# Performance work log

Measured on AMD Instinct MI355X. Metric: run time of the kernel, lower is better.

Reference implementation:

```python
import jax, jax.numpy as jnp
import numpy as np
from jax import lax

# Dims matching init_kwargs
T, BK, OBS = 2048, 64, 64   # obs_dim = percept_dim(63) + reward_dim(1)
H, P, N = 16, 64, 64        # nheads, headdim, d_state; d_inner = H*P = 1024
DIN = H * P


def setup_inputs() -> dict:
    key = jax.random.key(0)
    ks = jax.random.split(key, 12)
    s = lambda fan_in: 1.0 / np.sqrt(fan_in)
    return {
        "obs": jax.random.normal(ks[0], (T, BK, OBS), jnp.float32),
        "reward": jax.random.normal(ks[1], (T, BK, 1), jnp.float32),
        "W_in": jax.random.normal(ks[2], (OBS, DIN), jnp.float32) * s(OBS),
        "W_B": jax.random.normal(ks[3], (OBS, N), jnp.float32) * s(OBS),
        "W_C": jax.random.normal(ks[4], (OBS, N), jnp.float32) * s(OBS),
        "W_dt": jax.random.normal(ks[5], (1, H), jnp.float32),
        "dt_bias": jax.random.normal(ks[6], (H,), jnp.float32) * 0.5,
        "A_log": jax.random.uniform(ks[7], (H,), jnp.float32, 0.0, 1.0),
        "D": jax.random.normal(ks[8], (H,), jnp.float32),
        "W_out": jax.random.normal(ks[9], (DIN, 1), jnp.float32) * s(DIN),
        "init_state": jax.random.normal(ks[10], (H, P, N), jnp.float32) * 0.1,
        "k": 8,
    }


def reference(obs, reward, W_in, W_B, W_C, W_dt, dt_bias, A_log, D, W_out, init_state, k):
    # obs: (T, Bk, obs_dim), reward: (T, Bk, 1)
    Tn, Bk, _ = obs.shape
    # Precompute per-step projections (vectorized over time)
    u = (obs @ W_in).reshape(Tn, Bk, H, P)      # (T,Bk,H,P) input stream
    Bm = obs @ W_B                              # (T,Bk,N) input-dependent B
    Cm = obs @ W_C                              # (T,Bk,N) input-dependent C
    dt = jax.nn.softplus(reward @ W_dt + dt_bias)  # (T,Bk,H) reward-modulated dt
    A = -jnp.exp(A_log)                          # (H,) negative decay rates
    decay = jnp.exp(dt * A)                     # (T,Bk,H)

    # Cache init: zeros + initial_states (per QAgent.forward)
    h0 = jnp.broadcast_to(init_state, (Bk, H, P, N))

    def step(h, inp):
        u_t, B_t, C_t, dt_t, dec_t = inp
        # selective-scan state update: h = h*exp(dt*A) + dt*u (outer) B
        h = h * dec_t[..., None, None] + (dt_t[..., None] * u_t)[..., None] * B_t[:, None, None, :]
        y = jnp.einsum('bhpn,bn->bhp', h, C_t) + D[None, :, None] * u_t
        o = y.reshape(Bk, DIN) @ W_out          # (Bk, 1) scalar Q per option
        return h, o

    _, ys = lax.scan(step, h0, (u, Bm, Cm, dt, decay))  # ys: (T, Bk, 1)
    q = ys.reshape(Tn, -1, k)                   # (T, B, k)
    logits = q
    return q, logits
```

## Files before the change

kernel.cpp:

```cpp
#include <hip/hip_runtime.h>
#include <math.h>

#define TT     2048
#define BKK    64
#define OBSD   64
#define NH     16
#define PDIM   64
#define NSTATE 64
#define DINN   1024
#define TB     (TT*BKK)
#define DDS    32
#define BCS    128

template <int CTRL>
__device__ __forceinline__ float dpp_add(float x) {
    int y = __builtin_amdgcn_update_dpp(0, __float_as_int(x), CTRL, 0xF, 0xF, true);
    return x + __int_as_float(y);
}
__device__ __forceinline__ float wave_sum_lane63(float x) {
    x = dpp_add<0x111>(x);
    x = dpp_add<0x112>(x);
    x = dpp_add<0x114>(x);
    x = dpp_add<0x118>(x);
    x = dpp_add<0x142>(x);
    x = dpp_add<0x143>(x);
    return x;
}

__device__ __forceinline__ float softplusf(float z) {
    return (z > 20.f) ? z : log1pf(expf(z));
}

#define LOAD_DX(ptr, dd_, xx_)                                            \
    {                                                                     \
        const float4* _p = (const float4*)(ptr);                          \
        float4 a0 = _p[0], a1 = _p[1], a2 = _p[2], a3 = _p[3];            \
        float4 b0 = _p[4], b1 = _p[5], b2 = _p[6], b3 = _p[7];            \
        dd_[0]=a0.x; dd_[1]=a0.y; dd_[2]=a0.z; dd_[3]=a0.w;               \
        dd_[4]=a1.x; dd_[5]=a1.y; dd_[6]=a1.z; dd_[7]=a1.w;               \
        dd_[8]=a2.x; dd_[9]=a2.y; dd_[10]=a2.z; dd_[11]=a2.w;             \
        dd_[12]=a3.x; dd_[13]=a3.y; dd_[14]=a3.z; dd_[15]=a3.w;           \
        xx_[0]=b0.x; xx_[1]=b0.y; xx_[2]=b0.z; xx_[3]=b0.w;               \
        xx_[4]=b1.x; xx_[5]=b1.y; xx_[6]=b1.z; xx_[7]=b1.w;               \
        xx_[8]=b2.x; xx_[9]=b2.y; xx_[10]=b2.z; xx_[11]=b2.w;             \
        xx_[12]=b3.x; xx_[13]=b3.y; xx_[14]=b3.z; xx_[15]=b3.w;           \
    }

__global__ __launch_bounds__(256)
void init_proj2(const float* __restrict__ Win, const float* __restrict__ Wout,
                const float* __restrict__ initS,
                float* __restrict__ wproj, float* __restrict__ g0) {
    const int t = threadIdx.x;
    if (blockIdx.x < 4) {
        const int idx = blockIdx.x * 256 + t;
        const int k = idx >> 4, h = idx & 15;
        float s = 0.f;
#pragma unroll 8
        for (int p = 0; p < PDIM; ++p)
            s = fmaf(Win[(size_t)k * DINN + h * 64 + p], Wout[h * 64 + p], s);
        wproj[idx] = s;
    } else {
        const int idx = (blockIdx.x - 4) * 256 + t;
        const int h = idx >> 6, n = idx & 63;
        float s = 0.f;
#pragma unroll 8
        for (int p = 0; p < PDIM; ++p)
            s = fmaf(initS[h * PDIM * NSTATE + p * NSTATE + n], Wout[h * 64 + p], s);
        g0[idx] = s;
    }
}

__global__ __launch_bounds__(256)
void bc_gemm(const float* __restrict__ obs, const float* __restrict__ WB,
             const float* __restrict__ WC, float* __restrict__ BC) {
    __shared__ float tile[128 * OBSD];

    const int t = threadIdx.x;
    const size_t r0 = (size_t)blockIdx.x * 128;

    {
        const float4* src = (const float4*)(obs + r0 * OBSD);
        float4* dst = (float4*)tile;
#pragma unroll
        for (int i = 0; i < 8; ++i)
            dst[i * 256 + t] = src[i * 256 + t];
    }
    __syncthreads();

    const int lane = t & 63;
    const int w = __builtin_amdgcn_readfirstlane(t >> 6);

    float wb[64], wc[64];
#pragma unroll
    for (int k = 0; k < 64; ++k) wb[k] = WB[k * 64 + lane];
#pragma unroll
    for (int k = 0; k < 64; ++k) wc[k] = WC[k * 64 + lane];

    const float* trow = tile + w * 32 * OBSD;
    float* brow = BC + (r0 + w * 32) * BCS;

#pragma unroll 1
    for (int r = 0; r < 32; ++r) {
        const float4* tr4 = (const float4*)(trow + r * OBSD);
        float s0 = 0.f, s1 = 0.f, s2 = 0.f, s3 = 0.f;
        float c0 = 0.f, c1 = 0.f, c2 = 0.f, c3 = 0.f;
#pragma unroll
        for (int kq = 0; kq < 16; ++kq) {
            const float4 o = tr4[kq];
            const int k = kq * 4;
            s0 = fmaf(o.x, wb[k],     s0);  c0 = fmaf(o.x, wc[k],     c0);
            s1 = fmaf(o.y, wb[k + 1], s1);  c1 = fmaf(o.y, wc[k + 1], c1);
            s2 = fmaf(o.z, wb[k + 2], s2);  c2 = fmaf(o.z, wc[k + 2], c2);
            s3 = fmaf(o.w, wb[k + 3], s3);  c3 = fmaf(o.w, wc[k + 3], c3);
        }
        brow[lane]      = (s0 + s1) + (s2 + s3);
        brow[64 + lane] = (c0 + c1) + (c2 + c3);
        brow += BCS;
    }
}

__global__ __launch_bounds__(256)
void prelude3(const float* __restrict__ obs, const float* __restrict__ reward,
              const float* __restrict__ Wdt, const float* __restrict__ dtb,
              const float* __restrict__ Alog, const float* __restrict__ Dv,
              const float* __restrict__ wproj, float* __restrict__ dd,
              float* __restrict__ obw) {
    int gw = (blockIdx.x * 256 + threadIdx.x) >> 6;
    gw = __builtin_amdgcn_readfirstlane(gw);
    const int lane = threadIdx.x & 63;
    const int row0 = gw * 8;
    if (row0 >= TB) return;

    const int h = lane & 15;
    const int q = lane >> 4;

    const float wdt_h = Wdt[h];
    const float dtb_h = dtb[h];
    const float A_h   = -expf(Alog[h]);
    const float D_h   = Dv[h];
    float wpj[16];
#pragma unroll
    for (int j = 0; j < 16; ++j)
        wpj[j] = wproj[(q * 16 + j) * 16 + h];

#pragma unroll 1
    for (int r = 0; r < 8; ++r) {
        const int row = row0 + r;

        const float4* oq = (const float4*)(obs + (size_t)row * OBSD + q * 16);
        float4 o0 = oq[0], o1 = oq[1], o2 = oq[2], o3 = oq[3];
        float wpart = 0.f;
        wpart = fmaf(o0.x, wpj[0],  wpart); wpart = fmaf(o0.y, wpj[1],  wpart);
        wpart = fmaf(o0.z, wpj[2],  wpart); wpart = fmaf(o0.w, wpj[3],  wpart);
        wpart = fmaf(o1.x, wpj[4],  wpart); wpart = fmaf(o1.y, wpj[5],  wpart);
        wpart = fmaf(o1.z, wpj[6],  wpart); wpart = fmaf(o1.w, wpj[7],  wpart);
        wpart = fmaf(o2.x, wpj[8],  wpart); wpart = fmaf(o2.y, wpj[9],  wpart);
        wpart = fmaf(o2.z, wpj[10], wpart); wpart = fmaf(o2.w, wpj[11], wpart);
        wpart = fmaf(o3.x, wpj[12], wpart); wpart = fmaf(o3.y, wpj[13], wpart);
        wpart = fmaf(o3.z, wpj[14], wpart); wpart = fmaf(o3.w, wpj[15], wpart);
        wpart += __shfl_xor(wpart, 16, 64);
        wpart += __shfl_xor(wpart, 32, 64);

        const float rew  = reward[row];
        const float dtv  = softplusf(fmaf(rew, wdt_h, dtb_h));
        const float decv = expf(dtv * A_h);
        const float xwv  = dtv * wpart;

        float* dr = dd + (size_t)row * DDS;
        if (q == 0) dr[h]      = decv;
        if (q == 1) dr[16 + h] = xwv;

        float dw = D_h * wpart;
        dw += __shfl_xor(dw, 1, 64);
        dw += __shfl_xor(dw, 2, 64);
        dw += __shfl_xor(dw, 4, 64);
        dw += __shfl_xor(dw, 8, 64);
        if (lane == 0) obw[row] = dw;
    }
}

template <int NCT>
__global__ __launch_bounds__(256)
void phaseA(const float* __restrict__ BC, const float* __restrict__ dd,
            float* __restrict__ Send, float* __restrict__ Ptot) {
    const int CLT = TT / NCT;
    int w = blockIdx.x * 4 + (threadIdx.x >> 6);
    w = __builtin_amdgcn_readfirstlane(w);
    const int lane = threadIdx.x & 63;
    const int b = w & 63;
    const int c = w >> 6;

    const float* bp = BC + ((size_t)(c * CLT) * BKK + b) * BCS;
    const float* dr = dd + ((size_t)(c * CLT) * BKK + b) * DDS;

    float g[16], Pc[16];
#pragma unroll
    for (int hh = 0; hh < 16; ++hh) { g[hh] = 0.f; Pc[hh] = 1.f; }

    float Bv = bp[lane];
    float dec_[16], xw_[16];
    LOAD_DX(dr, dec_, xw_);

#pragma unroll 2
    for (int i = 0; i < CLT; ++i) {
        const float* bn = bp + (size_t)BKK * BCS;
        const float* dn = dr + (size_t)BKK * DDS;
        float Bn = 0.f;
        float decn_[16], xwn_[16];
        if (i < CLT - 1) {
            Bn = bn[lane];
            LOAD_DX(dn, decn_, xwn_);
        }
#pragma unroll
        for (int hh = 0; hh < 16; ++hh) {
            g[hh] = fmaf(g[hh], dec_[hh], xw_[hh] * Bv);
            Pc[hh] *= dec_[hh];
        }
        bp = bn; dr = dn; Bv = Bn;
        if (i < CLT - 1) {
#pragma unroll
            for (int hh = 0; hh < 16; ++hh) { dec_[hh] = decn_[hh]; xw_[hh] = xwn_[hh]; }
        }
    }

    const size_t base = ((size_t)c * BKK + b) * 16;
#pragma unroll
    for (int hh = 0; hh < 16; ++hh)
        Send[(base + hh) * 64 + lane] = g[hh];
    if (lane == 0) {
#pragma unroll
        for (int hh = 0; hh < 16; ++hh)
            Ptot[base + hh] = Pc[hh];
    }
}

template <int NCT>
__global__ __launch_bounds__(64)
void phaseB(const float* __restrict__ g0, const float* __restrict__ Send,
            const float* __restrict__ Ptot, float* __restrict__ gcbuf) {
    const int b    = blockIdx.x;
    const int lane = threadIdx.x;

    float g[16];
#pragma unroll
    for (int hh = 0; hh < 16; ++hh)
        g[hh] = g0[hh * 64 + lane];

    float S_[16], P_[16];
    {
        const size_t base = (size_t)b * 16;
#pragma unroll
        for (int hh = 0; hh < 16; ++hh) S_[hh] = Send[(base + hh) * 64 + lane];
        const float4* pp = (const float4*)(Ptot + base);
        float4 a0 = pp[0], a1 = pp[1], a2 = pp[2], a3 = pp[3];
        P_[0]=a0.x; P_[1]=a0.y; P_[2]=a0.z; P_[3]=a0.w;
        P_[4]=a1.x; P_[5]=a1.y; P_[6]=a1.z; P_[7]=a1.w;
        P_[8]=a2.x; P_[9]=a2.y; P_[10]=a2.z; P_[11]=a2.w;
        P_[12]=a3.x; P_[13]=a3.y; P_[14]=a3.z; P_[15]=a3.w;
    }

#pragma unroll 1
    for (int c = 0; c < NCT; ++c) {
        const size_t base = ((size_t)c * BKK + b) * 16;
        float Sn[16], Pn[16];
        if (c < NCT - 1) {
            const size_t nb = ((size_t)(c + 1) * BKK + b) * 16;
#pragma unroll
            for (int hh = 0; hh < 16; ++hh) Sn[hh] = Send[(nb + hh) * 64 + lane];
            const float4* pp = (const float4*)(Ptot + nb);
            float4 a0 = pp[0], a1 = pp[1], a2 = pp[2], a3 = pp[3];
            Pn[0]=a0.x; Pn[1]=a0.y; Pn[2]=a0.z; Pn[3]=a0.w;
            Pn[4]=a1.x; Pn[5]=a1.y; Pn[6]=a1.z; Pn[7]=a1.w;
            Pn[8]=a2.x; Pn[9]=a2.y; Pn[10]=a2.z; Pn[11]=a2.w;
            Pn[12]=a3.x; Pn[13]=a3.y; Pn[14]=a3.z; Pn[15]=a3.w;
        }
#pragma unroll
        for (int hh = 0; hh < 16; ++hh)
            gcbuf[(base + hh) * 64 + lane] = g[hh];
        if (c < NCT - 1) {
#pragma unroll
            for (int hh = 0; hh < 16; ++hh) {
                g[hh] = fmaf(P_[hh], g[hh], S_[hh]);
                P_[hh] = Pn[hh]; S_[hh] = Sn[hh];
            }
        }
    }
}

template <int NCT>
__global__ __launch_bounds__(256)
void phaseC(const float* __restrict__ BC, const float* __restrict__ dd,
            const float* __restrict__ obw, const float* __restrict__ gcbuf,
            float* __restrict__ qout) {
    const int CLT = TT / NCT;
    int w = blockIdx.x * 4 + (threadIdx.x >> 6);
    w = __builtin_amdgcn_readfirstlane(w);
    const int lane = threadIdx.x & 63;
    const int b = w & 63;
    const int c = w >> 6;

    const size_t sbase = ((size_t)c * BKK + b) * 16;
    float g[16];
#pragma unroll
    for (int hh = 0; hh < 16; ++hh)
        g[hh] = gcbuf[(sbase + hh) * 64 + lane];

    const float* bp = BC  + ((size_t)(c * CLT) * BKK + b) * BCS;
    const float* dr = dd  + ((size_t)(c * CLT) * BKK + b) * DDS;
    const float* op = obw + ((size_t)(c * CLT) * BKK + b);

    float Bv = bp[lane];
    float Cv = bp[64 + lane];
    float ob = op[0];
    float dec_[16], xw_[16];
    LOAD_DX(dr, dec_, xw_);

#pragma unroll 2
    for (int i = 0; i < CLT; ++i) {
        const float* bn = bp + (size_t)BKK * BCS;
        const float* dn = dr + (size_t)BKK * DDS;
        const float* on = op + (size_t)BKK;
        float Bn = 0.f, Cn = 0.f, obn = 0.f;
        float decn_[16], xwn_[16];
        if (i < CLT - 1) {
            Bn = bn[lane]; Cn = bn[64 + lane]; obn = on[0];
            LOAD_DX(dn, decn_, xwn_);
        }

        float y = 0.f;
#pragma unroll
        for (int hh = 0; hh < 16; ++hh) {
            g[hh] = fmaf(g[hh], dec_[hh], xw_[hh] * Bv);
            y = fmaf(g[hh], Cv, y);
        }

        float tot = wave_sum_lane63(y);
        if (lane == 63) {
            const size_t idx = (size_t)(c * CLT + i) * BKK + b;
            const float v = tot + ob;
            qout[idx]      = v;
            qout[TB + idx] = v;
        }

        bp = bn; dr = dn; op = on;
        Bv = Bn; Cv = Cn; ob = obn;
        if (i < CLT - 1) {
#pragma unroll
            for (int hh = 0; hh < 16; ++hh) { dec_[hh] = decn_[hh]; xw_[hh] = xwn_[hh]; }
        }
    }
}

extern "C" void kernel_launch(void* const* d_in, const int* in_sizes, int n_in,
                              void* d_out, int out_size, void* d_ws, size_t ws_size,
                              hipStream_t stream) {
    const float* obs    = (const float*)d_in[0];
    const float* reward = (const float*)d_in[1];
    const float* Win    = (const float*)d_in[2];
    const float* WB     = (const float*)d_in[3];
    const float* WC     = (const float*)d_in[4];
    const float* Wdt    = (const float*)d_in[5];
    const float* dtb    = (const float*)d_in[6];
    const float* Alog   = (const float*)d_in[7];
    const float* Dv     = (const float*)d_in[8];
    const float* Wout   = (const float*)d_in[9];
    const float* initS  = (const float*)d_in[10];
    float* qout = (float*)d_out;

    const size_t n_bc = (size_t)TB * BCS;
    const size_t n_dd = (size_t)TB * DDS;
    const size_t n_ob = (size_t)TB;

    float* BC    = (float*)d_ws;
    float* dd    = BC + n_bc;
    float* obw   = dd + n_dd;
    float* wproj = obw + n_ob;
    float* g0    = wproj + 1024;
    float* Send  = g0 + 1024;

    const size_t n_cs64 = (size_t)64 * BKK * 16 * 64;
    const size_t n_pt64 = (size_t)64 * BKK * 16;
    const size_t need64 = (n_bc + n_dd + n_ob + 2048 + 2 * n_cs64 + n_pt64) * 4;

    init_proj2<<<dim3(8), dim3(256), 0, stream>>>(Win, Wout, initS, wproj, g0);
    bc_gemm<<<dim3(TB / 128), dim3(256), 0, stream>>>(obs, WB, WC, BC);
    prelude3<<<dim3(TB / 32), dim3(256), 0, stream>>>(obs, reward, Wdt, dtb,
                                                      Alog, Dv, wproj, dd, obw);

    if (ws_size >= need64) {
        float* gcbuf = Send + n_cs64;
        float* Ptot  = gcbuf + n_cs64;
        phaseA<64><<<dim3(64 * 16), dim3(256), 0, stream>>>(BC, dd, Send, Ptot);
        phaseB<64><<<dim3(BKK), dim3(64), 0, stream>>>(g0, Send, Ptot, gcbuf);
        phaseC<64><<<dim3(64 * 16), dim3(256), 0, stream>>>(BC, dd, obw, gcbuf, qout);
    } else {
        const size_t n_cs32 = (size_t)32 * BKK * 16 * 64;
        float* gcbuf = Send + n_cs32;
        float* Ptot  = gcbuf + n_cs32;
        phaseA<32><<<dim3(32 * 16), dim3(256), 0, stream>>>(BC, dd, Send, Ptot);
        phaseB<32><<<dim3(BKK), dim3(64), 0, stream>>>(g0, Send, Ptot, gcbuf);
        phaseC<32><<<dim3(32 * 16), dim3(256), 0, stream>>>(BC, dd, obw, gcbuf, qout);
    }
}
```

Measured before the change: 280.7 us.

## Fuse B/C projection GEMM with dt/decay prelude and split B/C buffers

Merges the bc_gemm and prelude3 kernels into one proj_all kernel that stages a 64-row obs tile in shared memory once and reuses it for both the B/C projections and the dt/decay/wproj reductions. This removes one launch and one full re-read of obs from global memory. The B/C GEMM is restructured into a 16-row register-blocked loop over four k-chunks, so it holds far fewer weight registers and can run at higher occupancy via launch_bounds(256,4). B and C are now written to separate contiguous arrays instead of one interleaved 128-wide row, which changes the access stride in phaseA and phaseC.

```diff
diff --git a/kernel.cpp b/kernel.cpp
--- a/kernel.cpp
+++ b/kernel.cpp
@@ -10,7 +10,6 @@
 #define DINN   1024
 #define TB     (TT*BKK)
 #define DDS    32
-#define BCS    128
 
 template <int CTRL>
 __device__ __forceinline__ float dpp_add(float x) {
@@ -70,70 +69,74 @@
     }
 }
 
-__global__ __launch_bounds__(256)
-void bc_gemm(const float* __restrict__ obs, const float* __restrict__ WB,
-             const float* __restrict__ WC, float* __restrict__ BC) {
-    __shared__ float tile[128 * OBSD];
+__global__ __launch_bounds__(256, 4)
+void proj_all(const float* __restrict__ obs, const float* __restrict__ reward,
+              const float* __restrict__ WB, const float* __restrict__ WC,
+              const float* __restrict__ Wdt, const float* __restrict__ dtb,
+              const float* __restrict__ Alog, const float* __restrict__ Dv,
+              const float* __restrict__ wproj,
+              float* __restrict__ Bws, float* __restrict__ Cws,
+              float* __restrict__ dd, float* __restrict__ obw) {
+    __shared__ float tile[64 * OBSD];
 
     const int t = threadIdx.x;
-    const size_t r0 = (size_t)blockIdx.x * 128;
+    const size_t r0 = (size_t)blockIdx.x * 64;
 
     {
         const float4* src = (const float4*)(obs + r0 * OBSD);
         float4* dst = (float4*)tile;
 #pragma unroll
-        for (int i = 0; i < 8; ++i)
+        for (int i = 0; i < 4; ++i)
             dst[i * 256 + t] = src[i * 256 + t];
     }
     __syncthreads();
 
     const int lane = t & 63;
     const int w = __builtin_amdgcn_readfirstlane(t >> 6);
-
-    float wb[64], wc[64];
-#pragma unroll
-    for (int k = 0; k < 64; ++k) wb[k] = WB[k * 64 + lane];
-#pragma unroll
-    for (int k = 0; k < 64; ++k) wc[k] = WC[k * 64 + lane];
-
-    const float* trow = tile + w * 32 * OBSD;
-    float* brow = BC + (r0 + w * 32) * BCS;
+    const int rw = w * 16;
+
+    float accB[16], accC[16];
+#pragma unroll
+    for (int r = 0; r < 16; ++r) { accB[r] = 0.f; accC[r] = 0.f; }
 
 #pragma unroll 1
-    for (int r = 0; r < 32; ++r) {
-        const float4* tr4 = (const float4*)(trow + r * OBSD);
-        float s0 = 0.f, s1 = 0.f, s2 = 0.f, s3 = 0.f;
-        float c0 = 0.f, c1 = 0.f, c2 = 0.f, c3 = 0.f;
-#pragma unroll
-        for (int kq = 0; kq < 16; ++kq) {
-            const float4 o = tr4[kq];
-            const int k = kq * 4;
-            s0 = fmaf(o.x, wb[k],     s0);  c0 = fmaf(o.x, wc[k],     c0);
-            s1 = fmaf(o.y, wb[k + 1], s1);  c1 = fmaf(o.y, wc[k + 1], c1);
-            s2 = fmaf(o.z, wb[k + 2], s2);  c2 = fmaf(o.z, wc[k + 2], c2);
-            s3 = fmaf(o.w, wb[k + 3], s3);  c3 = fmaf(o.w, wc[k + 3], c3);
-        }
-        brow[lane]      = (s0 + s1) + (s2 + s3);
-        brow[64 + lane] = (c0 + c1) + (c2 + c3);
-        brow += BCS;
-    }
-}
-
-__global__ __launch_bounds__(256)
-void prelude3(const float* __restrict__ obs, const float* __restrict__ reward,
-              const float* __restrict__ Wdt, const float* __restrict__ dtb,
-              const float* __restrict__ Alog, const float* __restrict__ Dv,
-              const float* __restrict__ wproj, float* __restrict__ dd,
-              float* __restrict__ obw) {
-    int gw = (blockIdx.x * 256 + threadIdx.x) >> 6;
-    gw = __builtin_amdgcn_readfirstlane(gw);
-    const int lane = threadIdx.x & 63;
-    const int row0 = gw * 8;
-    if (row0 >= TB) return;
+    for (int kb = 0; kb < 4; ++kb) {
+        float wb[16], wc[16];
+#pragma unroll
+        for (int j = 0; j < 16; ++j) {
+            wb[j] = WB[(kb * 16 + j) * 64 + lane];
+            wc[j] = WC[(kb * 16 + j) * 64 + lane];
+        }
+#pragma unroll
+        for (int r = 0; r < 16; ++r) {
+            const float4* tp = (const float4*)(tile + (rw + r) * OBSD + kb * 16);
+            const float4 o0 = tp[0], o1 = tp[1], o2 = tp[2], o3 = tp[3];
+            accB[r] = fmaf(o0.x, wb[0],  accB[r]);  accC[r] = fmaf(o0.x, wc[0],  accC[r]);
+            accB[r] = fmaf(o0.y, wb[1],  accB[r]);  accC[r] = fmaf(o0.y, wc[1],  accC[r]);
+            accB[r] = fmaf(o0.z, wb[2],  accB[r]);  accC[r] = fmaf(o0.z, wc[2],  accC[r]);
+            accB[r] = fmaf(o0.w, wb[3],  accB[r]);  accC[r] = fmaf(o0.w, wc[3],  accC[r]);
+            accB[r] = fmaf(o1.x, wb[4],  accB[r]);  accC[r] = fmaf(o1.x, wc[4],  accC[r]);
+            accB[r] = fmaf(o1.y, wb[5],  accB[r]);  accC[r] = fmaf(o1.y, wc[5],  accC[r]);
+            accB[r] = fmaf(o1.z, wb[6],  accB[r]);  accC[r] = fmaf(o1.z, wc[6],  accC[r]);
+            accB[r] = fmaf(o1.w, wb[7],  accB[r]);  accC[r] = fmaf(o1.w, wc[7],  accC[r]);
+            accB[r] = fmaf(o2.x, wb[8],  accB[r]);  accC[r] = fmaf(o2.x, wc[8],  accC[r]);
+            accB[r] = fmaf(o2.y, wb[9],  accB[r]);  accC[r] = fmaf(o2.y, wc[9],  accC[r]);
+            accB[r] = fmaf(o2.z, wb[10], accB[r]);  accC[r] = fmaf(o2.z, wc[10], accC[r]);
+            accB[r] = fmaf(o2.w, wb[11], accB[r]);  accC[r] = fmaf(o2.w, wc[11], accC[r]);
+            accB[r] = fmaf(o3.x, wb[12], accB[r]);  accC[r] = fmaf(o3.x, wc[12], accC[r]);
+            accB[r] = fmaf(o3.y, wb[13], accB[r]);  accC[r] = fmaf(o3.y, wc[13], accC[r]);
+            accB[r] = fmaf(o3.z, wb[14], accB[r]);  accC[r] = fmaf(o3.z, wc[14], accC[r]);
+            accB[r] = fmaf(o3.w, wb[15], accB[r]);  accC[r] = fmaf(o3.w, wc[15], accC[r]);
+        }
+    }
+#pragma unroll
+    for (int r = 0; r < 16; ++r) {
+        Bws[(r0 + rw + r) * 64 + lane] = accB[r];
+        Cws[(r0 + rw + r) * 64 + lane] = accC[r];
+    }
 
     const int h = lane & 15;
     const int q = lane >> 4;
-
     const float wdt_h = Wdt[h];
     const float dtb_h = dtb[h];
     const float A_h   = -expf(Alog[h]);
@@ -144,11 +147,10 @@
         wpj[j] = wproj[(q * 16 + j) * 16 + h];
 
 #pragma unroll 1
-    for (int r = 0; r < 8; ++r) {
-        const int row = row0 + r;
-
-        const float4* oq = (const float4*)(obs + (size_t)row * OBSD + q * 16);
-        float4 o0 = oq[0], o1 = oq[1], o2 = oq[2], o3 = oq[3];
+    for (int r = 0; r < 16; ++r) {
+        const size_t row = r0 + rw + r;
+        const float4* tp = (const float4*)(tile + (rw + r) * OBSD + q * 16);
+        const float4 o0 = tp[0], o1 = tp[1], o2 = tp[2], o3 = tp[3];
         float wpart = 0.f;
         wpart = fmaf(o0.x, wpj[0],  wpart); wpart = fmaf(o0.y, wpj[1],  wpart);
         wpart = fmaf(o0.z, wpj[2],  wpart); wpart = fmaf(o0.w, wpj[3],  wpart);
@@ -166,7 +168,7 @@
         const float decv = expf(dtv * A_h);
         const float xwv  = dtv * wpart;
 
-        float* dr = dd + (size_t)row * DDS;
+        float* dr = dd + row * DDS;
         if (q == 0) dr[h]      = decv;
         if (q == 1) dr[16 + h] = xwv;
 
@@ -181,7 +183,7 @@
 
 template <int NCT>
 __global__ __launch_bounds__(256)
-void phaseA(const float* __restrict__ BC, const float* __restrict__ dd,
+void phaseA(const float* __restrict__ Bws, const float* __restrict__ dd,
             float* __restrict__ Send, float* __restrict__ Ptot) {
     const int CLT = TT / NCT;
     int w = blockIdx.x * 4 + (threadIdx.x >> 6);
@@ -190,8 +192,8 @@
     const int b = w & 63;
     const int c = w >> 6;
 
-    const float* bp = BC + ((size_t)(c * CLT) * BKK + b) * BCS;
-    const float* dr = dd + ((size_t)(c * CLT) * BKK + b) * DDS;
+    const float* bp = Bws + ((size_t)(c * CLT) * BKK + b) * 64;
+    const float* dr = dd  + ((size_t)(c * CLT) * BKK + b) * DDS;
 
     float g[16], Pc[16];
 #pragma unroll
@@ -203,7 +205,7 @@
 
 #pragma unroll 2
     for (int i = 0; i < CLT; ++i) {
-        const float* bn = bp + (size_t)BKK * BCS;
+        const float* bn = bp + (size_t)BKK * 64;
         const float* dn = dr + (size_t)BKK * DDS;
         float Bn = 0.f;
         float decn_[16], xwn_[16];
@@ -289,9 +291,9 @@
 
 template <int NCT>
 __global__ __launch_bounds__(256)
-void phaseC(const float* __restrict__ BC, const float* __restrict__ dd,
-            const float* __restrict__ obw, const float* __restrict__ gcbuf,
-            float* __restrict__ qout) {
+void phaseC(const float* __restrict__ Bws, const float* __restrict__ Cws,
+            const float* __restrict__ dd, const float* __restrict__ obw,
+            const float* __restrict__ gcbuf, float* __restrict__ qout) {
     const int CLT = TT / NCT;
     int w = blockIdx.x * 4 + (threadIdx.x >> 6);
     w = __builtin_amdgcn_readfirstlane(w);
@@ -305,25 +307,27 @@
     for (int hh = 0; hh < 16; ++hh)
         g[hh] = gcbuf[(sbase + hh) * 64 + lane];
 
-    const float* bp = BC  + ((size_t)(c * CLT) * BKK + b) * BCS;
+    const float* bp = Bws + ((size_t)(c * CLT) * BKK + b) * 64;
+    const float* cp = Cws + ((size_t)(c * CLT) * BKK + b) * 64;
     const float* dr = dd  + ((size_t)(c * CLT) * BKK + b) * DDS;
     const float* op = obw + ((size_t)(c * CLT) * BKK + b);
 
     float Bv = bp[lane];
-    float Cv = bp[64 + lane];
+    float Cv = cp[lane];
     float ob = op[0];
     float dec_[16], xw_[16];
     LOAD_DX(dr, dec_, xw_);
 
 #pragma unroll 2
     for (int i = 0; i < CLT; ++i) {
-        const float* bn = bp + (size_t)BKK * BCS;
+        const float* bn = bp + (size_t)BKK * 64;
+        const float* cn = cp + (size_t)BKK * 64;
         const float* dn = dr + (size_t)BKK * DDS;
         const float* on = op + (size_t)BKK;
         float Bn = 0.f, Cn = 0.f, obn = 0.f;
         float decn_[16], xwn_[16];
         if (i < CLT - 1) {
-            Bn = bn[lane]; Cn = bn[64 + lane]; obn = on[0];
+            Bn = bn[lane]; Cn = cn[lane]; obn = on[0];
             LOAD_DX(dn, decn_, xwn_);
         }
 
@@ -342,7 +346,7 @@
             qout[TB + idx] = v;
         }
 
-        bp = bn; dr = dn; op = on;
+        bp = bn; cp = cn; dr = dn; op = on;
         Bv = Bn; Cv = Cn; ob = obn;
         if (i < CLT - 1) {
 #pragma unroll
@@ -367,12 +371,13 @@
     const float* initS  = (const float*)d_in[10];
     float* qout = (float*)d_out;
 
-    const size_t n_bc = (size_t)TB * BCS;
+    const size_t n_B  = (size_t)TB * 64;
     const size_t n_dd = (size_t)TB * DDS;
     const size_t n_ob = (size_t)TB;
 
-    float* BC    = (float*)d_ws;
-    float* dd    = BC + n_bc;
+    float* Bws   = (float*)d_ws;
+    float* Cws   = Bws + n_B;
+    float* dd    = Cws + n_B;
     float* obw   = dd + n_dd;
     float* wproj = obw + n_ob;
     float* g0    = wproj + 1024;
@@ -380,25 +385,24 @@
 
     const size_t n_cs64 = (size_t)64 * BKK * 16 * 64;
     const size_t n_pt64 = (size_t)64 * BKK * 16;
-    const size_t need64 = (n_bc + n_dd + n_ob + 2048 + 2 * n_cs64 + n_pt64) * 4;
+    const size_t need64 = (2 * n_B + n_dd + n_ob + 2048 + 2 * n_cs64 + n_pt64) * 4;
 
     init_proj2<<<dim3(8), dim3(256), 0, stream>>>(Win, Wout, initS, wproj, g0);
-    bc_gemm<<<dim3(TB / 128), dim3(256), 0, stream>>>(obs, WB, WC, BC);
-    prelude3<<<dim3(TB / 32), dim3(256), 0, stream>>>(obs, reward, Wdt, dtb,
-                                                      Alog, Dv, wproj, dd, obw);
+    proj_all<<<dim3(TB / 64), dim3(256), 0, stream>>>(obs, reward, WB, WC, Wdt, dtb,
+                                                      Alog, Dv, wproj, Bws, Cws, dd, obw);
 
     if (ws_size >= need64) {
         float* gcbuf = Send + n_cs64;
         float* Ptot  = gcbuf + n_cs64;
-        phaseA<64><<<dim3(64 * 16), dim3(256), 0, stream>>>(BC, dd, Send, Ptot);
+        phaseA<64><<<dim3(64 * 16), dim3(256), 0, stream>>>(Bws, dd, Send, Ptot);
         phaseB<64><<<dim3(BKK), dim3(64), 0, stream>>>(g0, Send, Ptot, gcbuf);
-        phaseC<64><<<dim3(64 * 16), dim3(256), 0, stream>>>(BC, dd, obw, gcbuf, qout);
+        phaseC<64><<<dim3(64 * 16), dim3(256), 0, stream>>>(Bws, Cws, dd, obw, gcbuf, qout);
     } else {
         const size_t n_cs32 = (size_t)32 * BKK * 16 * 64;
         float* gcbuf = Send + n_cs32;
         float* Ptot  = gcbuf + n_cs32;
-        phaseA<32><<<dim3(32 * 16), dim3(256), 0, stream>>>(BC, dd, Send, Ptot);
+        phaseA<32><<<dim3(32 * 16), dim3(256), 0, stream>>>(Bws, dd, Send, Ptot);
         phaseB<32><<<dim3(BKK), dim3(64), 0, stream>>>(g0, Send, Ptot, gcbuf);
-        phaseC<32><<<dim3(32 * 16), dim3(256), 0, stream>>>(BC, dd, obw, gcbuf, qout);
-    }
-}
+        phaseC<32><<<dim3(32 * 16), dim3(256), 0, stream>>>(Bws, Cws, dd, obw, gcbuf, qout);
+    }
+}
```

New measurement: 255.1 us. -9.1%, faster.
